# Optimization experiments

Measured on AMD Instinct MI355X. Metric: run time of the kernel, lower is better.

Reference implementation:

```python
import jax, jax.numpy as jnp
import numpy as np
import math

B, S, H = 1, 2048, 4096
NH, HD = 32, 128  # heads, head_dim
ROPE_THETA = 10000.0
SINK = 4
RECENT_RATIO = 0.1


def setup_inputs() -> dict:
    key = jax.random.key(0)
    ks = jax.random.split(key, 5)
    scale = 0.02
    return {
        "hidden_states": jax.random.normal(ks[0], (B, S, H), jnp.float32),
        "Wq": jax.random.normal(ks[1], (H, H), jnp.float32) * scale,
        "Wk": jax.random.normal(ks[2], (H, H), jnp.float32) * scale,
        "Wv": jax.random.normal(ks[3], (H, H), jnp.float32) * scale,
        "Wo": jax.random.normal(ks[4], (H, H), jnp.float32) * scale,
        "position_ids": jnp.arange(S, dtype=jnp.int64)[None, :],
    }


def _rope(x, cos, sin):
    # x: [B, NH, S, HD]; rotate_half = cat(-x2, x1)
    half = x.shape[-1] // 2
    rot = jnp.concatenate([-x[..., half:], x[..., :half]], axis=-1)
    return x * cos + rot * sin


def reference(hidden_states, Wq, Wk, Wv, Wo, position_ids):
    b, s, h = hidden_states.shape
    # projections (torch Linear: x @ W^T), split heads -> [B, NH, S, HD]
    q = (hidden_states @ Wq.T).reshape(b, s, NH, HD).transpose(0, 2, 1, 3)
    k = (hidden_states @ Wk.T).reshape(b, s, NH, HD).transpose(0, 2, 1, 3)
    v = (hidden_states @ Wv.T).reshape(b, s, NH, HD).transpose(0, 2, 1, 3)

    # rotary embeddings from position_ids
    inv_freq = 1.0 / (ROPE_THETA ** (jnp.arange(0, HD, 2, dtype=jnp.float32) / HD))
    freqs = position_ids.astype(jnp.float32)[..., None] * inv_freq  # [B, S, HD/2]
    emb = jnp.concatenate([freqs, freqs], axis=-1)                   # [B, S, HD]
    cos = jnp.cos(emb)[:, None, :, :]
    sin = jnp.sin(emb)[:, None, :, :]
    q = _rope(q, cos, sin)
    k = _rope(k, cos, sin)

    # causal attention
    scores = jnp.einsum('bhqd,bhkd->bhqk', q, k) / math.sqrt(HD)
    neg = jnp.finfo(scores.dtype).min
    causal = jnp.tril(jnp.ones((s, s), dtype=bool))
    scores = jnp.where(causal[None, None], scores, neg)
    attn = jax.nn.softmax(scores, axis=-1)
    out = jnp.einsum('bhqk,bhkd->bhqd', attn, v)
    out = out.transpose(0, 2, 1, 3).reshape(b, s, h)
    attn_output = out @ Wo.T

    # H2O streaming cache eviction: sink (first 4) + recent window KV
    recent = int(s * RECENT_RATIO)
    k_evicted = jnp.concatenate([k[:, :, :SINK, :], k[:, :, s - recent:, :]], axis=2)
    v_evicted = jnp.concatenate([v[:, :, :SINK, :], v[:, :, s - recent:, :]], axis=2)
    return attn_output, k_evicted, v_evicted
```

## Files before the change

### kernel.cpp

```cpp
#include <hip/hip_runtime.h>
#include <hip/hip_bf16.h>

typedef __bf16 bf16;
typedef __bf16 bf16x4 __attribute__((ext_vector_type(4)));
typedef __bf16 bf16x8 __attribute__((ext_vector_type(8)));
typedef float f32x4 __attribute__((ext_vector_type(4)));

#define MFMA16(a, b, c) __builtin_amdgcn_mfma_f32_16x16x32_bf16(a, b, c, 0, 0, 0)

constexpr int S_LEN = 2048;
constexpr int HDIM = 4096;
constexpr int NHEADS = 32;
constexpr int HEADD = 128;
constexpr int SINKN = 4;
constexpr int RECENT = 204;
constexpr int EVROWS = SINKN + RECENT;
constexpr float QSCALE = 0.08838834764831845f;

constexpr int JOBS_PER_HEAD = 40;
constexpr int SLOTS_PER_HEAD = 36;
constexpr size_t SLOT_BYTES = 33792;

__device__ inline bf16x8 cvt8(const float* p) {
    float4 a = *(const float4*)p;
    float4 b = *(const float4*)(p + 4);
    return bf16x8{(bf16)a.x, (bf16)a.y, (bf16)a.z, (bf16)a.w,
                  (bf16)b.x, (bf16)b.y, (bf16)b.z, (bf16)b.w};
}

__device__ inline void gload16(const bf16* g, bf16* l) {
    __builtin_amdgcn_global_load_lds(
        (const __attribute__((address_space(1))) unsigned int*)g,
        (__attribute__((address_space(3))) unsigned int*)l, 16, 0, 0);
}

__global__ __launch_bounds__(256) void cvt_kernel(const float* __restrict__ in,
                                                  bf16* __restrict__ out, int n8) {
    int i = blockIdx.x * 256 + threadIdx.x;
    if (i >= n8) return;
    *(bf16x8*)(out + (size_t)i * 8) = cvt8(in + (size_t)i * 8);
}

__device__ __forceinline__ void stage_b256(const bf16* __restrict__ Bp, bf16* dst,
                                           int K, int kc, int tid) {
#pragma unroll
    for (int r = 0; r < 2; ++r) {
        int idx = r * 512 + tid;
        int row = idx >> 3;
        int gs = (idx & 7) ^ (row & 7);
        gload16(Bp + (size_t)row * K + kc + gs * 8, dst + idx * 8);
    }
}
template <int MH>
__device__ __forceinline__ void stage_a256(const bf16* __restrict__ Ap, bf16* dst,
                                           int K, int kc, int tid) {
#pragma unroll
    for (int r = 0; r < 2; ++r) {
        int idx = r * 512 + tid;
        int row = idx >> 3;
        int gs = (idx & 7) ^ (row & 7);
        gload16(Ap + (size_t)(MH * 128 + row) * K + kc + gs * 8,
                dst + MH * 8192 + idx * 8);
    }
}
template <int MH>
__device__ __forceinline__ void lda256(const bf16* buf, int wm, int lg, int lr,
                                       bf16x8 (&af)[2][2]) {
#pragma unroll
    for (int mt = 0; mt < 2; ++mt)
#pragma unroll
        for (int kk = 0; kk < 2; ++kk)
            af[mt][kk] = *(const bf16x8*)&buf[MH * 8192 + (wm * 32 + mt * 16 + lr) * 64 +
                                              (((kk * 4 + lg) ^ (lr & 7)) * 8)];
}
__device__ __forceinline__ void ldb256(const bf16* buf, int wn, int lg, int lr,
                                       bf16x8 (&bfr)[4][2]) {
#pragma unroll
    for (int nt = 0; nt < 4; ++nt)
#pragma unroll
        for (int kk = 0; kk < 2; ++kk)
            bfr[nt][kk] = *(const bf16x8*)&buf[(wn * 64 + nt * 16 + lr) * 64 +
                                               (((kk * 4 + lg) ^ (lr & 7)) * 8)];
}
template <int MH>
__device__ __forceinline__ void mma256(const bf16x8 (&af)[2][2], const bf16x8 (&bfr)[4][2],
                                       f32x4 (&acc)[2][2][4]) {
#pragma unroll
    for (int mt = 0; mt < 2; ++mt)
#pragma unroll
        for (int nt = 0; nt < 4; ++nt)
#pragma unroll
            for (int kk = 0; kk < 2; ++kk)
                acc[MH][mt][nt] = MFMA16(af[mt][kk], bfr[nt][kk], acc[MH][mt][nt]);
}

template <bool C_IS_F32>
__global__ __launch_bounds__(512, 2) void gemm256(const bf16* __restrict__ A,
                                                  const bf16* __restrict__ B,
                                                  void* __restrict__ Cv,
                                                  int M, int N, int K) {
    __shared__ bf16 Abuf[2][256 * 64];
    __shared__ bf16 Bbuf[2][128 * 64];

    const int tid = threadIdx.x;
    const int lane = tid & 63, wid = tid >> 6;
    const int wm = wid >> 1, wn = wid & 1;
    const int lg = lane >> 4, lr = lane & 15;

    const int bid = blockIdx.x;
    const int bx = (bid & 7) * 4 + (bid >> 6);
    const int by = (bid >> 3) & 7;
    const int m0 = by * 256, n0 = bx * 128;

    const bf16* Ap = A + (size_t)m0 * K;
    const bf16* Bp = B + (size_t)n0 * K;

    f32x4 acc[2][2][4] = {};
    bf16x8 af[2][2], bfr[4][2];

    stage_b256(Bp, Bbuf[0], K, 0, tid);
    stage_a256<0>(Ap, Abuf[0], K, 0, tid);
    stage_a256<1>(Ap, Abuf[0], K, 0, tid);
    asm volatile("s_waitcnt vmcnt(2)" ::: "memory");
    __builtin_amdgcn_s_barrier();

    const bf16 *Ard = Abuf[0], *Brd = Bbuf[0];
    bf16 *Awr = Abuf[1], *Bwr = Bbuf[1];

    const int NT = K / 64;
    for (int t = 0; t < NT - 1; ++t) {
        const int kc = (t + 1) * 64;
        ldb256(Brd, wn, lg, lr, bfr);
        lda256<0>(Ard, wm, lg, lr, af);
        stage_b256(Bp, Bwr, K, kc, tid);
        stage_a256<0>(Ap, Awr, K, kc, tid);
        __builtin_amdgcn_s_barrier();
        asm volatile("s_waitcnt lgkmcnt(0)" ::: "memory");
        __builtin_amdgcn_sched_barrier(0);
        __builtin_amdgcn_s_setprio(1);
        mma256<0>(af, bfr, acc);
        __builtin_amdgcn_s_setprio(0);
        asm volatile("s_waitcnt vmcnt(4)" ::: "memory");
        __builtin_amdgcn_s_barrier();
        lda256<1>(Ard, wm, lg, lr, af);
        stage_a256<1>(Ap, Awr, K, kc, tid);
        __builtin_amdgcn_s_barrier();
        asm volatile("s_waitcnt lgkmcnt(0)" ::: "memory");
        __builtin_amdgcn_sched_barrier(0);
        __builtin_amdgcn_s_setprio(1);
        mma256<1>(af, bfr, acc);
        __builtin_amdgcn_s_setprio(0);
        asm volatile("s_waitcnt vmcnt(2)" ::: "memory");
        __builtin_amdgcn_s_barrier();
        const bf16* tA = Ard; Ard = Awr; Awr = (bf16*)tA;
        const bf16* tB = Brd; Brd = Bwr; Bwr = (bf16*)tB;
    }
    asm volatile("s_waitcnt vmcnt(0)" ::: "memory");
    __builtin_amdgcn_s_barrier();
    ldb256(Brd, wn, lg, lr, bfr);
    lda256<0>(Ard, wm, lg, lr, af);
    mma256<0>(af, bfr, acc);
    lda256<1>(Ard, wm, lg, lr, af);
    mma256<1>(af, bfr, acc);

#pragma unroll
    for (int mh = 0; mh < 2; ++mh)
#pragma unroll
        for (int mt = 0; mt < 2; ++mt)
#pragma unroll
            for (int nt = 0; nt < 4; ++nt)
#pragma unroll
                for (int r = 0; r < 4; ++r) {
                    int row = m0 + mh * 128 + wm * 32 + mt * 16 + lg * 4 + r;
                    int col = n0 + wn * 64 + nt * 16 + lr;
                    if constexpr (C_IS_F32)
                        ((float*)Cv)[(size_t)row * N + col] = acc[mh][mt][nt][r];
                    else
                        ((bf16*)Cv)[(size_t)row * N + col] = (bf16)acc[mh][mt][nt][r];
                }
}

__global__ __launch_bounds__(256) void rope_kernel(bf16* __restrict__ q,
                                                   bf16* __restrict__ k) {
    const int s = blockIdx.x;
    const int t = threadIdx.x;
    const int hh = t >> 3;
    const int i0 = (t & 7) << 3;
    const size_t base = (size_t)s * HDIM + hh * HEADD;

    bf16x8 q1 = *(bf16x8*)(q + base + i0);
    bf16x8 q2 = *(bf16x8*)(q + base + 64 + i0);
    bf16x8 k1 = *(bf16x8*)(k + base + i0);
    bf16x8 k2 = *(bf16x8*)(k + base + 64 + i0);
    bf16x8 q1o, q2o, k1o, k2o;
    const float pos = (float)s;
#pragma unroll
    for (int j = 0; j < 8; ++j) {
        float f = pos * exp2f((float)(i0 + j) * (-0.2076205059304602f));
        float sn, cs;
        sincosf(f, &sn, &cs);
        float x1 = (float)q1[j], x2 = (float)q2[j];
        q1o[j] = (bf16)((x1 * cs - x2 * sn) * QSCALE);
        q2o[j] = (bf16)((x2 * cs + x1 * sn) * QSCALE);
        x1 = (float)k1[j]; x2 = (float)k2[j];
        k1o[j] = (bf16)(x1 * cs - x2 * sn);
        k2o[j] = (bf16)(x2 * cs + x1 * sn);
    }
    *(bf16x8*)(q + base + i0) = q1o;
    *(bf16x8*)(q + base + 64 + i0) = q2o;
    *(bf16x8*)(k + base + i0) = k1o;
    *(bf16x8*)(k + base + 64 + i0) = k2o;
}

__global__ __launch_bounds__(256) void transpose_v(const bf16* __restrict__ v,
                                                   bf16* __restrict__ vt) {
    __shared__ bf16 tile[64][136];
    const int h = blockIdx.x;
    const int s0 = blockIdx.y * 64;
    const int tid = threadIdx.x;
#pragma unroll
    for (int j = 0; j < 4; ++j) {
        int ch = tid + 256 * j;
        int row = ch >> 4, c8 = (ch & 15) << 3;
        *(bf16x8*)&tile[row][c8] =
            *(const bf16x8*)(v + (size_t)(s0 + row) * HDIM + h * HEADD + c8);
    }
    __syncthreads();
#pragma unroll
    for (int j = 0; j < 4; ++j) {
        int ch = tid + 256 * j;
        int d = ch >> 3, s8 = (ch & 7) << 3;
        bf16x8 w;
#pragma unroll
        for (int i = 0; i < 8; ++i) w[i] = tile[s8 + i][d];
        *(bf16x8*)(vt + ((size_t)h * HEADD + d) * S_LEN + s0 + s8) = w;
    }
}

__global__ __launch_bounds__(256, 3) void attn_kernel(const bf16* __restrict__ q,
                                                      const bf16* __restrict__ k,
                                                      const bf16* __restrict__ vt,
                                                      bf16* __restrict__ o,
                                                      char* __restrict__ partials) {
    __shared__ bf16 K_lds[64 * 128];
    __shared__ bf16 V_lds[128 * 64];
    __shared__ bf16 P_lds[4][32 * 72];

    const int tid = threadIdx.x;
    const int lane = tid & 63, wid = tid >> 6;
    const int lg = lane >> 4, lr = lane & 15;

    const int bj = blockIdx.x;
    const int h = bj / JOBS_PER_HEAD;
    const int within = JOBS_PER_HEAD - 1 - (bj % JOBS_PER_HEAD);
    int qb, chunk, nj;
    if (within < 4)       { qb = within; chunk = 0; nj = 1; }
    else if (within < 12) { int u = within - 4;  qb = 4  + (u >> 1); chunk = u & 1;        nj = 2; }
    else if (within < 24) { int u = within - 12; int q3 = u / 3; qb = 8 + q3; chunk = u - 3 * q3; nj = 3; }
    else                  { int u = within - 24; qb = 12 + (u >> 2); chunk = u & 3;        nj = 4; }
    const int q0 = qb * 128;
    const int ntiles = 2 * qb + 2;
    const int tb = chunk * 8;
    const int te = min(tb + 8, ntiles);

    bf16x8 aq[2][4];
#pragma unroll
    for (int rs = 0; rs < 2; ++rs)
#pragma unroll
        for (int dc = 0; dc < 4; ++dc)
            aq[rs][dc] = *(const bf16x8*)(q + (size_t)(q0 + wid * 32 + rs * 16 + lr) * HDIM +
                                          h * HEADD + dc * 32 + lg * 8);

    f32x4 oacc[2][8] = {};
    float m_[2] = {-1e30f, -1e30f};
    float l_[2] = {0.f, 0.f};
    bf16* pw = &P_lds[wid][0];

    for (int t = tb; t < te; ++t) {
        const int kv0 = t << 6;
#pragma unroll
        for (int i = 0; i < 4; ++i) {
            const int c = wid * 4 + i;
            const int krow = 4 * c + (lane >> 4);
            const int kg = (lane & 15) ^ (krow & 7);
            gload16(k + (size_t)(kv0 + krow) * HDIM + h * HEADD + kg * 8, &K_lds[c * 512]);
            const int vrow = 8 * c + (lane >> 3);
            const int vg = (lane & 7) ^ (vrow & 7);
            gload16(vt + (size_t)(h * HEADD + vrow) * S_LEN + kv0 + vg * 8, &V_lds[c * 512]);
        }
        __syncthreads();

        f32x4 st[2][4] = {};
#pragma unroll
        for (int kt = 0; kt < 4; ++kt) {
            bf16x8 kf[4];
#pragma unroll
            for (int dc = 0; dc < 4; ++dc)
                kf[dc] = *(const bf16x8*)&K_lds[(kt * 16 + lr) * 128 +
                                                (((dc * 4 + lg) ^ (lr & 7)) * 8)];
#pragma unroll
            for (int dc = 0; dc < 4; ++dc) {
                st[0][kt] = MFMA16(kf[dc], aq[0][dc], st[0][kt]);
                st[1][kt] = MFMA16(kf[dc], aq[1][dc], st[1][kt]);
            }
        }

#pragma unroll
        for (int rs = 0; rs < 2; ++rs) {
            const int qr0 = q0 + wid * 32 + rs * 16;
            const int qidx = qr0 + lr;
            const bool nm = (kv0 + 63) > qr0;
            float v[16];
#pragma unroll
            for (int kt = 0; kt < 4; ++kt)
#pragma unroll
                for (int r = 0; r < 4; ++r) {
                    float x = st[rs][kt][r];
                    if (nm && (kv0 + kt * 16 + lg * 4 + r > qidx)) x = -1e30f;
                    v[kt * 4 + r] = x;
                }
            float pm = v[0];
#pragma unroll
            for (int i = 1; i < 16; ++i) pm = fmaxf(pm, v[i]);
            pm = fmaxf(pm, __shfl_xor(pm, 16));
            pm = fmaxf(pm, __shfl_xor(pm, 32));

            if (__any(pm > m_[rs] + 8.0f)) {
                float mn = fmaxf(m_[rs], pm);
                float sc = __expf(m_[rs] - mn);
                m_[rs] = mn;
                l_[rs] *= sc;
                float scb[4];
#pragma unroll
                for (int r = 0; r < 4; ++r)
                    scb[r] = __uint_as_float(__builtin_amdgcn_ds_bpermute(
                        (lg * 4 + r) * 4, __float_as_uint(sc)));
#pragma unroll
                for (int dt = 0; dt < 8; ++dt)
#pragma unroll
                    for (int r = 0; r < 4; ++r) oacc[rs][dt][r] *= scb[r];
            }
            const float mn = m_[rs];
            float rsum = 0.f;
#pragma unroll
            for (int kt = 0; kt < 4; ++kt) {
                bf16x4 pk;
#pragma unroll
                for (int r = 0; r < 4; ++r) {
                    float p = __expf(v[kt * 4 + r] - mn);
                    rsum += p;
                    pk[r] = (bf16)p;
                }
                *(bf16x4*)&pw[(rs * 16 + lr) * 72 + kt * 16 + lg * 4] = pk;
            }
            rsum += __shfl_xor(rsum, 16);
            rsum += __shfl_xor(rsum, 32);
            l_[rs] += rsum;
        }

        bf16x8 pa[2][2];
#pragma unroll
        for (int rs = 0; rs < 2; ++rs)
#pragma unroll
            for (int kt2 = 0; kt2 < 2; ++kt2)
                pa[rs][kt2] = *(const bf16x8*)&pw[(rs * 16 + lr) * 72 + kt2 * 32 + lg * 8];
#pragma unroll
        for (int kt2 = 0; kt2 < 2; ++kt2)
#pragma unroll
            for (int dt = 0; dt < 8; ++dt) {
                bf16x8 bv = *(const bf16x8*)&V_lds[(dt * 16 + lr) * 64 +
                                                   (((kt2 * 4 + lg) ^ (lr & 7)) * 8)];
                oacc[0][dt] = MFMA16(pa[0][kt2], bv, oacc[0][dt]);
                oacc[1][dt] = MFMA16(pa[1][kt2], bv, oacc[1][dt]);
            }
        __syncthreads();
    }

    if (nj == 1) {
#pragma unroll
        for (int rs = 0; rs < 2; ++rs) {
            float lb[4];
#pragma unroll
            for (int r = 0; r < 4; ++r)
                lb[r] = __uint_as_float(__builtin_amdgcn_ds_bpermute(
                    (lg * 4 + r) * 4, __float_as_uint(l_[rs])));
#pragma unroll
            for (int r = 0; r < 4; ++r) {
                float inv = 1.0f / lb[r];
                const int row = q0 + wid * 32 + rs * 16 + lg * 4 + r;
#pragma unroll
                for (int dt = 0; dt < 8; ++dt)
                    o[(size_t)row * HDIM + h * HEADD + dt * 16 + lr] =
                        (bf16)(oacc[rs][dt][r] * inv);
            }
        }
    } else {
        const int sb = (qb < 8) ? (qb - 4) * 2 : (qb < 12) ? 8 + (qb - 8) * 3
                                                           : 20 + (qb - 12) * 4;
        char* slotp = partials + ((size_t)h * SLOTS_PER_HEAD + sb + chunk) * SLOT_BYTES;
        bf16* Op = (bf16*)slotp;
        float* mp = (float*)(slotp + 32768);
        float* lp = mp + 128;
#pragma unroll
        for (int rs = 0; rs < 2; ++rs) {
            const int rowl = wid * 32 + rs * 16;
#pragma unroll
            for (int r = 0; r < 4; ++r)
#pragma unroll
                for (int dt = 0; dt < 8; ++dt)
                    Op[(rowl + lg * 4 + r) * HEADD + dt * 16 + lr] = (bf16)oacc[rs][dt][r];
            if (lg == 0) { mp[rowl + lr] = m_[rs]; lp[rowl + lr] = l_[rs]; }
        }
    }
}

__global__ __launch_bounds__(256) void combine_kernel(const char* __restrict__ partials,
                                                      bf16* __restrict__ o) {
    const int h = blockIdx.x;
    const int qb = 4 + blockIdx.y;
    const int nj = (2 * qb + 9) / 8;
    const int sb = (qb < 8) ? (qb - 4) * 2 : (qb < 12) ? 8 + (qb - 8) * 3
                                                       : 20 + (qb - 12) * 4;
    const char* base = partials + ((size_t)h * SLOTS_PER_HEAD + sb) * SLOT_BYTES;

    const int row = threadIdx.x >> 1;
    const int d0 = (threadIdx.x & 1) * 64;

    float mc[4], lc[4];
    float M = -1e30f;
    for (int c = 0; c < nj; ++c) {
        const char* sp = base + (size_t)c * SLOT_BYTES;
        mc[c] = ((const float*)(sp + 32768))[row];
        lc[c] = ((const float*)(sp + 33280))[row];
        M = fmaxf(M, mc[c]);
    }
    float denom = 0.f;
    float acc[64] = {};
    for (int c = 0; c < nj; ++c) {
        float wgt = __expf(mc[c] - M);
        denom += wgt * lc[c];
        const bf16* Op = (const bf16*)(base + (size_t)c * SLOT_BYTES);
#pragma unroll
        for (int j = 0; j < 8; ++j) {
            bf16x8 a = *(const bf16x8*)&Op[row * HEADD + d0 + j * 8];
#pragma unroll
            for (int e = 0; e < 8; ++e) acc[j * 8 + e] += wgt * (float)a[e];
        }
    }
    float inv = 1.0f / denom;
    bf16* dst = o + (size_t)(qb * 128 + row) * HDIM + h * HEADD + d0;
#pragma unroll
    for (int j = 0; j < 8; ++j) {
        bf16x8 w;
#pragma unroll
        for (int e = 0; e < 8; ++e) w[e] = (bf16)(acc[j * 8 + e] * inv);
        *(bf16x8*)&dst[j * 8] = w;
    }
}

__global__ __launch_bounds__(256) void evict_kernel(const bf16* __restrict__ k,
                                                    const bf16* __restrict__ v,
                                                    float* __restrict__ out) {
    const int total = NHEADS * EVROWS * HEADD;
    int idx = blockIdx.x * 256 + threadIdx.x;
    if (idx >= 2 * total) return;
    const int which = idx / total;
    const int rem = idx % total;
    const int hh = rem / (EVROWS * HEADD);
    const int i = (rem / HEADD) % EVROWS;
    const int d = rem % HEADD;
    const int s = (i < SINKN) ? i : (S_LEN - RECENT) + (i - SINKN);
    const bf16* src = which ? v : k;
    out[(size_t)S_LEN * HDIM + (size_t)which * total + rem] =
        (float)src[(size_t)s * HDIM + hh * HEADD + d];
}

extern "C" void kernel_launch(void* const* d_in, const int* in_sizes, int n_in,
                              void* d_out, int out_size, void* d_ws, size_t ws_size,
                              hipStream_t stream) {
    const float* hs = (const float*)d_in[0];
    const float* Wq = (const float*)d_in[1];
    const float* Wk = (const float*)d_in[2];
    const float* Wv = (const float*)d_in[3];
    const float* Wo = (const float*)d_in[4];
    float* out = (float*)d_out;

    const size_t MB = 1024 * 1024;
    char* w = (char*)d_ws;
    bf16* hs_bf = (bf16*)(w);
    bf16* W_bf  = (bf16*)(w + 16 * MB);
    char* part  = w;
    bf16* q_ws  = (bf16*)(w + 48 * MB);
    bf16* k_ws  = (bf16*)(w + 64 * MB);
    bf16* v_ws  = (bf16*)(w + 80 * MB);
    bf16* vt_ws = (bf16*)(w + 96 * MB);
    bf16* o_ws  = q_ws;

    const int nW8 = HDIM * HDIM / 8;
    const int nH8 = S_LEN * HDIM / 8;

    cvt_kernel<<<(nH8 + 255) / 256, 256, 0, stream>>>(hs, hs_bf, nH8);

    cvt_kernel<<<(nW8 + 255) / 256, 256, 0, stream>>>(Wq, W_bf, nW8);
    gemm256<false><<<256, 512, 0, stream>>>(hs_bf, W_bf, q_ws, S_LEN, HDIM, HDIM);
    cvt_kernel<<<(nW8 + 255) / 256, 256, 0, stream>>>(Wk, W_bf, nW8);
    gemm256<false><<<256, 512, 0, stream>>>(hs_bf, W_bf, k_ws, S_LEN, HDIM, HDIM);
    cvt_kernel<<<(nW8 + 255) / 256, 256, 0, stream>>>(Wv, W_bf, nW8);
    gemm256<false><<<256, 512, 0, stream>>>(hs_bf, W_bf, v_ws, S_LEN, HDIM, HDIM);

    rope_kernel<<<S_LEN, 256, 0, stream>>>(q_ws, k_ws);
    transpose_v<<<dim3(NHEADS, S_LEN / 64), 256, 0, stream>>>(v_ws, vt_ws);

    evict_kernel<<<(2 * NHEADS * EVROWS * HEADD + 255) / 256, 256, 0, stream>>>(k_ws, v_ws, out);

    attn_kernel<<<NHEADS * JOBS_PER_HEAD, 256, 0, stream>>>(q_ws, k_ws, vt_ws, o_ws, part);
    combine_kernel<<<dim3(NHEADS, 12), 256, 0, stream>>>(part, o_ws);

    cvt_kernel<<<(nW8 + 255) / 256, 256, 0, stream>>>(Wo, W_bf, nW8);
    gemm256<true><<<256, 512, 0, stream>>>(o_ws, W_bf, out, S_LEN, HDIM, HDIM);
}
```

Before: 511.3 us.

## Double-buffer K tiles and split V wait in attention loop

```diff
diff --git a/kernel.cpp b/kernel.cpp
--- a/kernel.cpp
+++ b/kernel.cpp
@@ -237,12 +237,12 @@
     }
 }
 
-__global__ __launch_bounds__(256, 3) void attn_kernel(const bf16* __restrict__ q,
+__global__ __launch_bounds__(256, 2) void attn_kernel(const bf16* __restrict__ q,
                                                       const bf16* __restrict__ k,
                                                       const bf16* __restrict__ vt,
                                                       bf16* __restrict__ o,
                                                       char* __restrict__ partials) {
-    __shared__ bf16 K_lds[64 * 128];
+    __shared__ bf16 K_lds[2][64 * 128];
     __shared__ bf16 V_lds[128 * 64];
     __shared__ bf16 P_lds[4][32 * 72];
 
@@ -255,9 +255,9 @@
     const int within = JOBS_PER_HEAD - 1 - (bj % JOBS_PER_HEAD);
     int qb, chunk, nj;
     if (within < 4)       { qb = within; chunk = 0; nj = 1; }
-    else if (within < 12) { int u = within - 4;  qb = 4  + (u >> 1); chunk = u & 1;        nj = 2; }
-    else if (within < 24) { int u = within - 12; int q3 = u / 3; qb = 8 + q3; chunk = u - 3 * q3; nj = 3; }
-    else                  { int u = within - 24; qb = 12 + (u >> 2); chunk = u & 3;        nj = 4; }
+    else if (within < 12) { int u2 = within - 4;  qb = 4  + (u2 >> 1); chunk = u2 & 1;        nj = 2; }
+    else if (within < 24) { int u2 = within - 12; int q3 = u2 / 3; qb = 8 + q3; chunk = u2 - 3 * q3; nj = 3; }
+    else                  { int u2 = within - 24; qb = 12 + (u2 >> 2); chunk = u2 & 3;        nj = 4; }
     const int q0 = qb * 128;
     const int ntiles = 2 * qb + 2;
     const int tb = chunk * 8;
@@ -276,28 +276,55 @@
     float l_[2] = {0.f, 0.f};
     bf16* pw = &P_lds[wid][0];
 
-    for (int t = tb; t < te; ++t) {
-        const int kv0 = t << 6;
+    {
+        const int kv0 = tb << 6;
 #pragma unroll
         for (int i = 0; i < 4; ++i) {
             const int c = wid * 4 + i;
             const int krow = 4 * c + (lane >> 4);
             const int kg = (lane & 15) ^ (krow & 7);
-            gload16(k + (size_t)(kv0 + krow) * HDIM + h * HEADD + kg * 8, &K_lds[c * 512]);
+            gload16(k + (size_t)(kv0 + krow) * HDIM + h * HEADD + kg * 8,
+                    &K_lds[0][c * 512]);
+        }
+    }
+
+    int cur = 0;
+    for (int t = tb; t < te; ++t) {
+        const int kv0 = t << 6;
+#pragma unroll
+        for (int i = 0; i < 4; ++i) {
+            const int c = wid * 4 + i;
             const int vrow = 8 * c + (lane >> 3);
             const int vg = (lane & 7) ^ (vrow & 7);
-            gload16(vt + (size_t)(h * HEADD + vrow) * S_LEN + kv0 + vg * 8, &V_lds[c * 512]);
-        }
-        __syncthreads();
-
+            gload16(vt + (size_t)(h * HEADD + vrow) * S_LEN + kv0 + vg * 8,
+                    &V_lds[c * 512]);
+        }
+        if (t + 1 < te) {
+            const int kvn = (t + 1) << 6;
+#pragma unroll
+            for (int i = 0; i < 4; ++i) {
+                const int c = wid * 4 + i;
+                const int krow = 4 * c + (lane >> 4);
+                const int kg = (lane & 15) ^ (krow & 7);
+                gload16(k + (size_t)(kvn + krow) * HDIM + h * HEADD + kg * 8,
+                        &K_lds[cur ^ 1][c * 512]);
+            }
+            asm volatile("s_waitcnt vmcnt(8)" ::: "memory");
+        } else {
+            asm volatile("s_waitcnt vmcnt(4)" ::: "memory");
+        }
+        __builtin_amdgcn_s_barrier();
+        __builtin_amdgcn_sched_barrier(0);
+
+        const bf16* Kb = &K_lds[cur][0];
         f32x4 st[2][4] = {};
 #pragma unroll
         for (int kt = 0; kt < 4; ++kt) {
             bf16x8 kf[4];
 #pragma unroll
             for (int dc = 0; dc < 4; ++dc)
-                kf[dc] = *(const bf16x8*)&K_lds[(kt * 16 + lr) * 128 +
-                                                (((dc * 4 + lg) ^ (lr & 7)) * 8)];
+                kf[dc] = *(const bf16x8*)&Kb[(kt * 16 + lr) * 128 +
+                                             (((dc * 4 + lg) ^ (lr & 7)) * 8)];
 #pragma unroll
             for (int dc = 0; dc < 4; ++dc) {
                 st[0][kt] = MFMA16(kf[dc], aq[0][dc], st[0][kt]);
@@ -358,6 +385,11 @@
             l_[rs] += rsum;
         }
 
+        if (t + 1 < te) asm volatile("s_waitcnt vmcnt(4)" ::: "memory");
+        else            asm volatile("s_waitcnt vmcnt(0)" ::: "memory");
+        __builtin_amdgcn_s_barrier();
+        __builtin_amdgcn_sched_barrier(0);
+
         bf16x8 pa[2][2];
 #pragma unroll
         for (int rs = 0; rs < 2; ++rs)
@@ -373,7 +405,10 @@
                 oacc[0][dt] = MFMA16(pa[0][kt2], bv, oacc[0][dt]);
                 oacc[1][dt] = MFMA16(pa[1][kt2], bv, oacc[1][dt]);
             }
-        __syncthreads();
+
+        __builtin_amdgcn_s_barrier();
+        __builtin_amdgcn_sched_barrier(0);
+        cur ^= 1;
     }
 
     if (nj == 1) {
```

Result: faster. 443.5 us (-13.3%).
